# Kernel optimization log

Hardware: AMD Instinct MI355X
Metric: run time of the kernel (lower is better)

## Reference

```python
import jax, jax.numpy as jnp
import numpy as np

B, S, D = 4, 2048, 1024
H, HD = 16, 64
WINDOW = 128


def setup_inputs() -> dict:
    key = jax.random.key(0)
    ks = jax.random.split(key, 8)
    scale = 1.0 / np.sqrt(D)
    return {
        "hidden_states": jax.random.normal(ks[0], (B, S, D), dtype=jnp.float32),
        "attention_mask": jnp.zeros((B, 1, 1, S), dtype=jnp.float32),
        "Wq": jax.random.normal(ks[1], (D, D), dtype=jnp.float32) * scale,
        "bq": jnp.zeros((D,), dtype=jnp.float32),
        "Wk": jax.random.normal(ks[2], (D, D), dtype=jnp.float32) * scale,
        "bk": jnp.zeros((D,), dtype=jnp.float32),
        "Wv": jax.random.normal(ks[3], (D, D), dtype=jnp.float32) * scale,
        "bv": jnp.zeros((D,), dtype=jnp.float32),
    }


def _proj(x, W, b):
    # [b t D] -> [b h t d]
    p = x @ W.T + b
    return p.reshape(x.shape[0], x.shape[1], H, HD).transpose(0, 2, 1, 3)


def reference(hidden_states, attention_mask, Wq, bq, Wk, bk, Wv, bv):
    q = _proj(hidden_states, Wq, bq)  # [b h t d]
    k = _proj(hidden_states, Wk, bk)
    v = _proj(hidden_states, Wv, bv)

    scores = jnp.einsum("bhtd,bhsd->bhts", q, k) / np.sqrt(HD)  # [b h t s]
    pos = jnp.arange(S)
    i, j = pos[:, None], pos[None, :]
    # causal (j <= i) AND sliding window (i - j <= w)
    allowed = (j <= i) & ((i - j) <= WINDOW)  # [t s]
    scores = jnp.where(allowed[None, None], scores, -jnp.inf)
    scores = scores + attention_mask  # additive padding mask [b,1,1,s]
    probs = jax.nn.softmax(scores, axis=-1)  # dropout identity in eval
    ctx = jnp.einsum("bhts,bhsd->bhtd", probs, v)
    return ctx.transpose(0, 2, 1, 3).reshape(B, S, D)
```

## Files before the change

kernel.cpp:

```cpp
#include <hip/hip_runtime.h>
#include <cstdint>

#define BDIM 4
#define SEQ 2048
#define DMODEL 1024
#define NH 16
#define HDIM 64

typedef __attribute__((ext_vector_type(8))) short bf16x8;
typedef __attribute__((ext_vector_type(4))) float f32x4;
typedef __attribute__((ext_vector_type(4))) int i32x4;
typedef __attribute__((ext_vector_type(4))) unsigned short u16x4;

#define MFMA16(a, b, c) __builtin_amdgcn_mfma_f32_16x16x32_bf16(a, b, c, 0, 0, 0)

__device__ __forceinline__ unsigned short f2bf(float x) {
    unsigned int u = __float_as_uint(x);
    unsigned int r = (u + 0x7FFFu + ((u >> 16) & 1u)) >> 16;
    return (unsigned short)r;
}

__device__ __forceinline__ void gload16(const void* g, void* l) {
    __builtin_amdgcn_global_load_lds(
        (const __attribute__((address_space(1))) unsigned int*)g,
        (__attribute__((address_space(3))) unsigned int*)l, 16, 0, 0);
}

__global__ __launch_bounds__(256) void k_cvt_x(const float* __restrict__ src,
                                               unsigned short* __restrict__ dst) {
    int i = blockIdx.x * 256 + threadIdx.x;
    float4 v = ((const float4*)src)[i];
    u16x4 o = {f2bf(v.x), f2bf(v.y), f2bf(v.z), f2bf(v.w)};
    ((u16x4*)dst)[i] = o;
}

__global__ __launch_bounds__(256) void k_cvt_w(const float* __restrict__ wq,
                                               const float* __restrict__ wk,
                                               const float* __restrict__ wv,
                                               unsigned short* __restrict__ dst) {
    int i = blockIdx.x * 256 + threadIdx.x;
    int e = i << 2;
    int which = e >> 20;
    int off = e & 0xFFFFF;
    const float* s = which == 0 ? wq : (which == 1 ? wk : wv);
    float4 v = *(const float4*)(s + off);
    u16x4 o = {f2bf(v.x), f2bf(v.y), f2bf(v.z), f2bf(v.w)};
    ((u16x4*)dst)[i] = o;
}

__global__ __launch_bounds__(256) void k_qkv(const unsigned short* __restrict__ X,
                                             const unsigned short* __restrict__ W,
                                             const float* __restrict__ bq,
                                             const float* __restrict__ bk,
                                             const float* __restrict__ bv,
                                             unsigned short* __restrict__ Qo,
                                             unsigned short* __restrict__ Ko,
                                             unsigned short* __restrict__ Vo) {
    __shared__ unsigned short ldsA[128 * 32];
    __shared__ unsigned short ldsB[128 * 32];
    const int tid = threadIdx.x;
    const int lane = tid & 63, wid = tid >> 6;
    const int wm = wid >> 1, wn = wid & 1;
    const int l15 = lane & 15, g = lane >> 4;
    const int m0 = blockIdx.y * 128, n0 = blockIdx.x * 128;

    f32x4 acc[4][4];
#pragma unroll
    for (int i = 0; i < 4; ++i)
#pragma unroll
        for (int j = 0; j < 4; ++j) acc[i][j] = (f32x4){0.f, 0.f, 0.f, 0.f};

    for (int kt = 0; kt < 32; ++kt) {
        const int k0 = kt << 5;
        __syncthreads();
#pragma unroll
        for (int it = 0; it < 2; ++it) {
            const int c = it * 256 + tid;
            const int row = c >> 2, sl = c & 3;
            gload16(X + (size_t)(m0 + row) * DMODEL + k0 + sl * 8, (char*)ldsA + c * 16);
            gload16(W + (size_t)(n0 + row) * DMODEL + k0 + sl * 8, (char*)ldsB + c * 16);
        }
        __syncthreads();
        bf16x8 a[4], b[4];
#pragma unroll
        for (int f = 0; f < 4; ++f) {
            a[f] = *(const bf16x8*)((const char*)ldsA + (wm * 64 + f * 16 + l15) * 64 + g * 16);
            b[f] = *(const bf16x8*)((const char*)ldsB + (wn * 64 + f * 16 + l15) * 64 + g * 16);
        }
#pragma unroll
        for (int fm = 0; fm < 4; ++fm)
#pragma unroll
            for (int fn = 0; fn < 4; ++fn) acc[fm][fn] = MFMA16(a[fm], b[fn], acc[fm][fn]);
    }

#pragma unroll
    for (int fn = 0; fn < 4; ++fn) {
        const int col = n0 + wn * 64 + fn * 16 + l15;
        const int proj = col >> 10, rem = col & 1023;
        const int h = rem >> 6, hd = rem & 63;
        const float* bp = proj == 0 ? bq : (proj == 1 ? bk : bv);
        const float bias = bp[rem];
        const float scl = (proj == 0) ? 0.125f : 1.0f;
        unsigned short* dst = proj == 0 ? Qo : (proj == 1 ? Ko : Vo);
#pragma unroll
        for (int fm = 0; fm < 4; ++fm) {
#pragma unroll
            for (int r = 0; r < 4; ++r) {
                const int m = m0 + wm * 64 + fm * 16 + g * 4 + r;
                const int bb = m >> 11, s = m & 2047;
                dst[(size_t)((bb * NH + h) * SEQ + s) * HDIM + hd] =
                    f2bf((acc[fm][fn][r] + bias) * scl);
            }
        }
    }
}

__global__ __launch_bounds__(256) void k_trv(const unsigned short* __restrict__ V,
                                             unsigned short* __restrict__ Vt) {
    __shared__ unsigned short tl[64][80];
    const int bh = blockIdx.y, s0 = blockIdx.x * 64;
    const int tid = threadIdx.x;
#pragma unroll
    for (int it = 0; it < 2; ++it) {
        const int c = it * 256 + tid;
        const int sl = c >> 3, hs = c & 7;
        i32x4 v = *(const i32x4*)(V + (size_t)(bh * SEQ + s0 + sl) * HDIM + hs * 8);
        union { i32x4 v; unsigned short u[8]; } uu;
        uu.v = v;
#pragma unroll
        for (int j = 0; j < 8; ++j) tl[hs * 8 + j][sl] = uu.u[j];
    }
    __syncthreads();
#pragma unroll
    for (int it = 0; it < 2; ++it) {
        const int c = it * 256 + tid;
        const int hd = c >> 3, ss = c & 7;
        i32x4 o = *(const i32x4*)(&tl[hd][ss * 8]);
        *(i32x4*)(Vt + (size_t)(bh * HDIM + hd) * SEQ + s0 + ss * 8) = o;
    }
}

__global__ __launch_bounds__(256) void k_attn(const unsigned short* __restrict__ Qg,
                                              const unsigned short* __restrict__ Kg,
                                              const unsigned short* __restrict__ Vtg,
                                              const float* __restrict__ amask,
                                              float* __restrict__ out) {
    __shared__ unsigned short kl[224 * 64];
    __shared__ unsigned short vl[64 * 224];
    __shared__ unsigned short pl[4 * 512];
    const int bid = blockIdx.x;
    const int bh = bid >> 5, qb = bid & 31;
    const int b = bh >> 4, h = bh & 15;
    const int q0 = qb << 6;
    const int kstart = q0 - 144;
    const int tid = threadIdx.x, lane = tid & 63, w = tid >> 6;
    const int l15 = lane & 15, g = lane >> 4;

#pragma unroll
    for (int it = 0; it < 7; ++it) {
        const int c = it * 256 + tid;
        {
            const int row = c >> 3, sl = c & 7;
            const int key = kstart + row;
            i32x4 v = {0, 0, 0, 0};
            if ((unsigned)key < (unsigned)SEQ)
                v = *(const i32x4*)(Kg + (size_t)(bh * SEQ + key) * HDIM + sl * 8);
            *(i32x4*)((char*)kl + ((row * 128 + sl * 16) ^ ((row & 7) << 4))) = v;
        }
        {
            const int row = c / 28, sl = c - row * 28;
            const int key0 = kstart + sl * 8;
            i32x4 v = {0, 0, 0, 0};
            if ((unsigned)key0 < (unsigned)SEQ)
                v = *(const i32x4*)(Vtg + (size_t)(bh * HDIM + row) * SEQ + key0);
            *(i32x4*)((char*)vl + ((row * 448 + sl * 16) ^ ((row & 7) << 4))) = v;
        }
    }
    const int iq = q0 + w * 16 + l15;
    const bf16x8 qf0 = *(const bf16x8*)(Qg + (size_t)(bh * SEQ + iq) * HDIM + g * 8);
    const bf16x8 qf1 = *(const bf16x8*)(Qg + (size_t)(bh * SEQ + iq) * HDIM + 32 + g * 8);
    __syncthreads();

    f32x4 acc[4];
#pragma unroll
    for (int i = 0; i < 4; ++i) acc[i] = (f32x4){0.f, 0.f, 0.f, 0.f};
    float m_run = -3.0e38f, l_run = 0.0f;
    char* pbase = (char*)pl + w * 1024;
    const int swq = (l15 & 7) << 4;

    for (int t = 0; t < 5; ++t) {
        const int tloc = w * 16 + t * 32;
        bf16x8 kf[2][2];
#pragma unroll
        for (int m = 0; m < 2; ++m) {
            const int row = tloc + m * 16 + l15;
            const int swz = (row & 7) << 4;
            kf[m][0] = *(const bf16x8*)((const char*)kl + ((row * 128 + g * 16) ^ swz));
            kf[m][1] = *(const bf16x8*)((const char*)kl + ((row * 128 + 64 + g * 16) ^ swz));
        }
        f32x4 sa0 = {0.f, 0.f, 0.f, 0.f}, sa1 = {0.f, 0.f, 0.f, 0.f};
        sa0 = MFMA16(kf[0][0], qf0, sa0);
        sa0 = MFMA16(kf[0][1], qf1, sa0);
        sa1 = MFMA16(kf[1][0], qf0, sa1);
        sa1 = MFMA16(kf[1][1], qf1, sa1);

        float mv[8];
#pragma unroll
        for (int f = 0; f < 2; ++f) {
            const int jb = kstart + tloc + f * 16 + g * 4;
            float4 m4 = {0.f, 0.f, 0.f, 0.f};
            if ((unsigned)jb < (unsigned)SEQ) m4 = *(const float4*)(amask + b * SEQ + jb);
            mv[f * 4 + 0] = m4.x; mv[f * 4 + 1] = m4.y;
            mv[f * 4 + 2] = m4.z; mv[f * 4 + 3] = m4.w;
        }
        float sv[8];
#pragma unroll
        for (int f = 0; f < 2; ++f) {
#pragma unroll
            for (int r = 0; r < 4; ++r) {
                const int jg = kstart + tloc + f * 16 + g * 4 + r;
                const float s = (f == 0 ? sa0[r] : sa1[r]) + mv[f * 4 + r];
                const bool ok = (jg >= 0) && (jg <= iq) && (iq - jg <= 128);
                sv[f * 4 + r] = ok ? s : -3.0e38f;
            }
        }
        float lm = sv[0];
#pragma unroll
        for (int i = 1; i < 8; ++i) lm = fmaxf(lm, sv[i]);
        lm = fmaxf(lm, __shfl_xor(lm, 16));
        lm = fmaxf(lm, __shfl_xor(lm, 32));
        const float m_new = fmaxf(m_run, lm);
        float p[8], alpha;
        if (m_new > -1.0e37f) {
            alpha = exp2f((m_run - m_new) * 1.44269504f);
#pragma unroll
            for (int i = 0; i < 8; ++i) p[i] = exp2f((sv[i] - m_new) * 1.44269504f);
        } else {
            alpha = 1.0f;
#pragma unroll
            for (int i = 0; i < 8; ++i) p[i] = 0.0f;
        }
        float rs = 0.f;
#pragma unroll
        for (int i = 0; i < 8; ++i) rs += p[i];
        rs += __shfl_xor(rs, 16);
        rs += __shfl_xor(rs, 32);
        l_run = l_run * alpha + rs;
        m_run = m_new;

        float a4[4];
#pragma unroll
        for (int r = 0; r < 4; ++r) a4[r] = __shfl(alpha, g * 4 + r);
#pragma unroll
        for (int fn = 0; fn < 4; ++fn) {
            f32x4 av = acc[fn];
            av[0] *= a4[0]; av[1] *= a4[1]; av[2] *= a4[2]; av[3] *= a4[3];
            acc[fn] = av;
        }
#pragma unroll
        for (int f = 0; f < 2; ++f) {
            u16x4 pu = {f2bf(p[f * 4 + 0]), f2bf(p[f * 4 + 1]),
                        f2bf(p[f * 4 + 2]), f2bf(p[f * 4 + 3])};
            *(u16x4*)(pbase + ((l15 * 64 + f * 32 + g * 8) ^ swq)) = pu;
        }
        asm volatile("s_waitcnt lgkmcnt(0)" ::: "memory");
        const bf16x8 pf = *(const bf16x8*)(pbase + ((l15 * 64 + g * 16) ^ swq));
#pragma unroll
        for (int fn = 0; fn < 4; ++fn) {
            const int vrow = fn * 16 + l15;
            const bf16x8 vf = *(const bf16x8*)((const char*)vl +
                ((vrow * 448 + tloc * 2 + g * 16) ^ ((vrow & 7) << 4)));
            acc[fn] = MFMA16(pf, vf, acc[fn]);
        }
    }
    float linv[4];
#pragma unroll
    for (int r = 0; r < 4; ++r) linv[r] = 1.0f / __shfl(l_run, g * 4 + r);
#pragma unroll
    for (int fn = 0; fn < 4; ++fn) {
#pragma unroll
        for (int r = 0; r < 4; ++r) {
            const int qrow = q0 + w * 16 + g * 4 + r;
            out[(size_t)(b * SEQ + qrow) * DMODEL + h * HDIM + fn * 16 + l15] =
                acc[fn][r] * linv[r];
        }
    }
}

extern "C" void kernel_launch(void* const* d_in, const int* in_sizes, int n_in,
                              void* d_out, int out_size, void* d_ws, size_t ws_size,
                              hipStream_t stream) {
    const float* hs = (const float*)d_in[0];
    const float* amask = (const float*)d_in[1];
    const float* wq = (const float*)d_in[2];
    const float* bq = (const float*)d_in[3];
    const float* wk = (const float*)d_in[4];
    const float* bk = (const float*)d_in[5];
    const float* wv = (const float*)d_in[6];
    const float* bv = (const float*)d_in[7];
    float* out = (float*)d_out;

    char* p = (char*)d_ws;
    unsigned short* Xbf = (unsigned short*)p;
    unsigned short* Wbf = (unsigned short*)(p + 16777216);
    unsigned short* Qb = (unsigned short*)(p + 16777216 + 6291456);
    unsigned short* Kb = Qb + 8388608;
    unsigned short* Vb = Kb + 8388608;
    unsigned short* Vtb = Xbf;

    k_cvt_x<<<8192, 256, 0, stream>>>(hs, Xbf);
    k_cvt_w<<<3072, 256, 0, stream>>>(wq, wk, wv, Wbf);
    k_qkv<<<dim3(24, 64), 256, 0, stream>>>(Xbf, Wbf, bq, bk, bv, Qb, Kb, Vb);
    k_trv<<<dim3(32, 64), 256, 0, stream>>>(Vb, Vtb);
    k_attn<<<2048, 256, 0, stream>>>(Qb, Kb, Vtb, amask, out);
}
```

Before: 145.9 us.

## Fuse V transpose into QKV epilogue and use single-pass softmax in attention

The QKV GEMM epilogue now writes V directly in transposed [b,h,d,s] layout, which removes the separate transpose kernel and its extra round trip through global memory. The attention kernel drops the online softmax. It computes all 40 scores per lane first, takes one max and one sum, writes the full P tile to LDS, and then runs the PV MFMAs in a separate loop. Block IDs are remapped so that neighbouring blocks land on different XCDs, and s_setprio is raised around the MFMA sections. The costs are higher register pressure from the 40-score array and a larger LDS footprint for P.

After: 131.5 us. 1.11x faster.

```diff
diff --git a/kernel.cpp b/kernel.cpp
--- a/kernel.cpp
+++ b/kernel.cpp
@@ -55,7 +55,7 @@
                                              const float* __restrict__ bv,
                                              unsigned short* __restrict__ Qo,
                                              unsigned short* __restrict__ Ko,
-                                             unsigned short* __restrict__ Vo) {
+                                             unsigned short* __restrict__ Vt) {
     __shared__ unsigned short ldsA[128 * 32];
     __shared__ unsigned short ldsB[128 * 32];
     const int tid = threadIdx.x;
@@ -100,43 +100,29 @@
         const int h = rem >> 6, hd = rem & 63;
         const float* bp = proj == 0 ? bq : (proj == 1 ? bk : bv);
         const float bias = bp[rem];
-        const float scl = (proj == 0) ? 0.125f : 1.0f;
-        unsigned short* dst = proj == 0 ? Qo : (proj == 1 ? Ko : Vo);
-#pragma unroll
-        for (int fm = 0; fm < 4; ++fm) {
-#pragma unroll
-            for (int r = 0; r < 4; ++r) {
-                const int m = m0 + wm * 64 + fm * 16 + g * 4 + r;
-                const int bb = m >> 11, s = m & 2047;
-                dst[(size_t)((bb * NH + h) * SEQ + s) * HDIM + hd] =
-                    f2bf((acc[fm][fn][r] + bias) * scl);
+        if (proj == 2) {
+#pragma unroll
+            for (int fm = 0; fm < 4; ++fm) {
+                const int mb = m0 + wm * 64 + fm * 16 + g * 4;
+                const int bb = mb >> 11, s = mb & 2047;
+                u16x4 ov = {f2bf(acc[fm][fn][0] + bias), f2bf(acc[fm][fn][1] + bias),
+                            f2bf(acc[fm][fn][2] + bias), f2bf(acc[fm][fn][3] + bias)};
+                *(u16x4*)(Vt + (size_t)((bb * NH + h) * HDIM + hd) * SEQ + s) = ov;
             }
-        }
-    }
-}
-
-__global__ __launch_bounds__(256) void k_trv(const unsigned short* __restrict__ V,
-                                             unsigned short* __restrict__ Vt) {
-    __shared__ unsigned short tl[64][80];
-    const int bh = blockIdx.y, s0 = blockIdx.x * 64;
-    const int tid = threadIdx.x;
-#pragma unroll
-    for (int it = 0; it < 2; ++it) {
-        const int c = it * 256 + tid;
-        const int sl = c >> 3, hs = c & 7;
-        i32x4 v = *(const i32x4*)(V + (size_t)(bh * SEQ + s0 + sl) * HDIM + hs * 8);
-        union { i32x4 v; unsigned short u[8]; } uu;
-        uu.v = v;
-#pragma unroll
-        for (int j = 0; j < 8; ++j) tl[hs * 8 + j][sl] = uu.u[j];
-    }
-    __syncthreads();
-#pragma unroll
-    for (int it = 0; it < 2; ++it) {
-        const int c = it * 256 + tid;
-        const int hd = c >> 3, ss = c & 7;
-        i32x4 o = *(const i32x4*)(&tl[hd][ss * 8]);
-        *(i32x4*)(Vt + (size_t)(bh * HDIM + hd) * SEQ + s0 + ss * 8) = o;
+        } else {
+            const float scl = (proj == 0) ? 0.125f : 1.0f;
+            unsigned short* dst = proj == 0 ? Qo : Ko;
+#pragma unroll
+            for (int fm = 0; fm < 4; ++fm) {
+#pragma unroll
+                for (int r = 0; r < 4; ++r) {
+                    const int m = m0 + wm * 64 + fm * 16 + g * 4 + r;
+                    const int bb = m >> 11, s = m & 2047;
+                    dst[(size_t)((bb * NH + h) * SEQ + s) * HDIM + hd] =
+                        f2bf((acc[fm][fn][r] + bias) * scl);
+                }
+            }
+        }
     }
 }
 
@@ -147,8 +133,9 @@
                                               float* __restrict__ out) {
     __shared__ unsigned short kl[224 * 64];
     __shared__ unsigned short vl[64 * 224];
-    __shared__ unsigned short pl[4 * 512];
-    const int bid = blockIdx.x;
+    __shared__ unsigned short pl[4 * 16 * 160];
+    const int bid0 = blockIdx.x;
+    const int bid = (bid0 & 7) * 256 + (bid0 >> 3);
     const int bh = bid >> 5, qb = bid & 31;
     const int b = bh >> 4, h = bh & 15;
     const int q0 = qb << 6;
@@ -181,13 +168,12 @@
     const bf16x8 qf1 = *(const bf16x8*)(Qg + (size_t)(bh * SEQ + iq) * HDIM + 32 + g * 8);
     __syncthreads();
 
-    f32x4 acc[4];
-#pragma unroll
-    for (int i = 0; i < 4; ++i) acc[i] = (f32x4){0.f, 0.f, 0.f, 0.f};
-    float m_run = -3.0e38f, l_run = 0.0f;
-    char* pbase = (char*)pl + w * 1024;
+    char* pbase = (char*)pl + w * 5120;
     const int swq = (l15 & 7) << 4;
-
+    float s[40];
+
+    __builtin_amdgcn_s_setprio(1);
+#pragma unroll
     for (int t = 0; t < 5; ++t) {
         const int tloc = w * 16 + t * 32;
         bf16x8 kf[2][2];
@@ -203,68 +189,68 @@
         sa0 = MFMA16(kf[0][1], qf1, sa0);
         sa1 = MFMA16(kf[1][0], qf0, sa1);
         sa1 = MFMA16(kf[1][1], qf1, sa1);
-
-        float mv[8];
 #pragma unroll
         for (int f = 0; f < 2; ++f) {
             const int jb = kstart + tloc + f * 16 + g * 4;
             float4 m4 = {0.f, 0.f, 0.f, 0.f};
             if ((unsigned)jb < (unsigned)SEQ) m4 = *(const float4*)(amask + b * SEQ + jb);
-            mv[f * 4 + 0] = m4.x; mv[f * 4 + 1] = m4.y;
-            mv[f * 4 + 2] = m4.z; mv[f * 4 + 3] = m4.w;
-        }
-        float sv[8];
+            const float mvv[4] = {m4.x, m4.y, m4.z, m4.w};
+#pragma unroll
+            for (int r = 0; r < 4; ++r) {
+                const int jg = jb + r;
+                const float sc = (f == 0 ? sa0[r] : sa1[r]) + mvv[r];
+                const bool ok = (jg >= 0) && (jg <= iq) && (iq - jg <= 128);
+                s[t * 8 + f * 4 + r] = ok ? sc : -3.0e38f;
+            }
+        }
+    }
+    __builtin_amdgcn_s_setprio(0);
+
+    float tr[20];
+#pragma unroll
+    for (int i = 0; i < 20; ++i) tr[i] = fmaxf(s[i], s[i + 20]);
+#pragma unroll
+    for (int i = 0; i < 10; ++i) tr[i] = fmaxf(tr[i], tr[i + 10]);
+#pragma unroll
+    for (int i = 0; i < 5; ++i) tr[i] = fmaxf(tr[i], tr[i + 5]);
+    float m = fmaxf(fmaxf(tr[0], tr[1]), fmaxf(tr[2], fmaxf(tr[3], tr[4])));
+    m = fmaxf(m, __shfl_xor(m, 16));
+    m = fmaxf(m, __shfl_xor(m, 32));
+
+    float ls0 = 0.f, ls1 = 0.f, ls2 = 0.f, ls3 = 0.f;
+#pragma unroll
+    for (int i = 0; i < 40; i += 4) {
+        float p0 = exp2f((s[i + 0] - m) * 1.44269504f);
+        float p1 = exp2f((s[i + 1] - m) * 1.44269504f);
+        float p2 = exp2f((s[i + 2] - m) * 1.44269504f);
+        float p3 = exp2f((s[i + 3] - m) * 1.44269504f);
+        s[i + 0] = p0; s[i + 1] = p1; s[i + 2] = p2; s[i + 3] = p3;
+        ls0 += p0; ls1 += p1; ls2 += p2; ls3 += p3;
+    }
+    float l = (ls0 + ls1) + (ls2 + ls3);
+    l += __shfl_xor(l, 16);
+    l += __shfl_xor(l, 32);
+
+#pragma unroll
+    for (int t = 0; t < 5; ++t) {
 #pragma unroll
         for (int f = 0; f < 2; ++f) {
-#pragma unroll
-            for (int r = 0; r < 4; ++r) {
-                const int jg = kstart + tloc + f * 16 + g * 4 + r;
-                const float s = (f == 0 ? sa0[r] : sa1[r]) + mv[f * 4 + r];
-                const bool ok = (jg >= 0) && (jg <= iq) && (iq - jg <= 128);
-                sv[f * 4 + r] = ok ? s : -3.0e38f;
-            }
-        }
-        float lm = sv[0];
-#pragma unroll
-        for (int i = 1; i < 8; ++i) lm = fmaxf(lm, sv[i]);
-        lm = fmaxf(lm, __shfl_xor(lm, 16));
-        lm = fmaxf(lm, __shfl_xor(lm, 32));
-        const float m_new = fmaxf(m_run, lm);
-        float p[8], alpha;
-        if (m_new > -1.0e37f) {
-            alpha = exp2f((m_run - m_new) * 1.44269504f);
-#pragma unroll
-            for (int i = 0; i < 8; ++i) p[i] = exp2f((sv[i] - m_new) * 1.44269504f);
-        } else {
-            alpha = 1.0f;
-#pragma unroll
-            for (int i = 0; i < 8; ++i) p[i] = 0.0f;
-        }
-        float rs = 0.f;
-#pragma unroll
-        for (int i = 0; i < 8; ++i) rs += p[i];
-        rs += __shfl_xor(rs, 16);
-        rs += __shfl_xor(rs, 32);
-        l_run = l_run * alpha + rs;
-        m_run = m_new;
-
-        float a4[4];
-#pragma unroll
-        for (int r = 0; r < 4; ++r) a4[r] = __shfl(alpha, g * 4 + r);
-#pragma unroll
-        for (int fn = 0; fn < 4; ++fn) {
-            f32x4 av = acc[fn];
-            av[0] *= a4[0]; av[1] *= a4[1]; av[2] *= a4[2]; av[3] *= a4[3];
-            acc[fn] = av;
-        }
-#pragma unroll
-        for (int f = 0; f < 2; ++f) {
-            u16x4 pu = {f2bf(p[f * 4 + 0]), f2bf(p[f * 4 + 1]),
-                        f2bf(p[f * 4 + 2]), f2bf(p[f * 4 + 3])};
-            *(u16x4*)(pbase + ((l15 * 64 + f * 32 + g * 8) ^ swq)) = pu;
-        }
-        asm volatile("s_waitcnt lgkmcnt(0)" ::: "memory");
-        const bf16x8 pf = *(const bf16x8*)(pbase + ((l15 * 64 + g * 16) ^ swq));
+            u16x4 pu = {f2bf(s[t * 8 + f * 4 + 0]), f2bf(s[t * 8 + f * 4 + 1]),
+                        f2bf(s[t * 8 + f * 4 + 2]), f2bf(s[t * 8 + f * 4 + 3])};
+            *(u16x4*)(pbase + ((l15 * 320 + t * 64 + f * 32 + g * 8) ^ swq)) = pu;
+        }
+    }
+    asm volatile("s_waitcnt lgkmcnt(0)" ::: "memory");
+    __builtin_amdgcn_sched_barrier(0);
+
+    f32x4 acc[4];
+#pragma unroll
+    for (int i = 0; i < 4; ++i) acc[i] = (f32x4){0.f, 0.f, 0.f, 0.f};
+    __builtin_amdgcn_s_setprio(1);
+#pragma unroll
+    for (int t = 0; t < 5; ++t) {
+        const int tloc = w * 16 + t * 32;
+        const bf16x8 pf = *(const bf16x8*)(pbase + ((l15 * 320 + t * 64 + g * 16) ^ swq));
 #pragma unroll
         for (int fn = 0; fn < 4; ++fn) {
             const int vrow = fn * 16 + l15;
@@ -273,9 +259,11 @@
             acc[fn] = MFMA16(pf, vf, acc[fn]);
         }
     }
+    __builtin_amdgcn_s_setprio(0);
+
     float linv[4];
 #pragma unroll
-    for (int r = 0; r < 4; ++r) linv[r] = 1.0f / __shfl(l_run, g * 4 + r);
+    for (int r = 0; r < 4; ++r) linv[r] = 1.0f / __shfl(l, g * 4 + r);
 #pragma unroll
     for (int fn = 0; fn < 4; ++fn) {
 #pragma unroll
@@ -303,14 +291,12 @@
     char* p = (char*)d_ws;
     unsigned short* Xbf = (unsigned short*)p;
     unsigned short* Wbf = (unsigned short*)(p + 16777216);
-    unsigned short* Qb = (unsigned short*)(p + 16777216 + 6291456);
+    unsigned short* Vtb = (unsigned short*)(p + 16777216 + 6291456);
+    unsigned short* Qb = Vtb + 8388608;
     unsigned short* Kb = Qb + 8388608;
-    unsigned short* Vb = Kb + 8388608;
-    unsigned short* Vtb = Xbf;
 
     k_cvt_x<<<8192, 256, 0, stream>>>(hs, Xbf);
     k_cvt_w<<<3072, 256, 0, stream>>>(wq, wk, wv, Wbf);
-    k_qkv<<<dim3(24, 64), 256, 0, stream>>>(Xbf, Wbf, bq, bk, bv, Qb, Kb, Vb);
-    k_trv<<<dim3(32, 64), 256, 0, stream>>>(Vb, Vtb);
+    k_qkv<<<dim3(24, 64), 256, 0, stream>>>(Xbf, Wbf, bq, bk, bv, Qb, Kb, Vtb);
     k_attn<<<2048, 256, 0, stream>>>(Qb, Kb, Vtb, amask, out);
 }
```
